# Kernel tuning notes

Measured on AMD Instinct MI355X. Metric: run time of the kernel, lower is better.

Reference implementation:

```python
import jax, jax.numpy as jnp
import numpy as np

TOP_K_PERCENT = 0.7


def setup_inputs() -> dict:
    key = jax.random.key(0)
    k1, k2, k3, k4 = jax.random.split(key, 4)
    B, C, H, W = 4, 19, 512, 1024
    logits = jax.random.normal(k1, (B, C, H, W), dtype=jnp.float32)
    labels = jax.random.randint(k2, (B, H, W), 0, C, dtype=jnp.int64)
    smooth_labels = jax.random.uniform(k3, (B, C, H, W), dtype=jnp.float32)
    weight2 = jax.random.uniform(k4, (C,), dtype=jnp.float32)
    return {"logits": logits, "labels": labels, "smooth_labels": smooth_labels, "weight2": weight2}


def reference(logits, labels, smooth_labels, weight2):
    # Fused equivalent of the per-class loop:
    #   cum[b,h,w] = sum_c smooth[b,c,h,w] * weight2[c] * (-log_softmax(logits)[b,c,h,w])
    # (ignore_label=-1 never matches any class index, so no masking occurs.)
    logp = jax.nn.log_softmax(logits, axis=1)  # [B,C,H,W]
    w = weight2[None, :, None, None]
    pixel_losses_2 = -(smooth_labels * w * logp).sum(axis=1)  # [B,H,W]
    flat = pixel_losses_2.reshape(-1)
    k = int(TOP_K_PERCENT * flat.shape[0])  # static shape -> python int
    top_vals, _ = jax.lax.top_k(flat, k)
    return top_vals.mean()
```

## Files before the change

### kernel.cpp

```cpp
#include <hip/hip_runtime.h>

#define NPIX 2097152
#define NT2  1048576
#define NT4  524288
#define NCH  19
#define CPL2 262144
#define KSEL 1468006u
#define LBLK 4096
#define HB   512
#define H1B  4096
#define H2B  1024

#define OFF_COMB1 (NPIX*4)
#define OFF_COMB2 (OFF_COMB1 + H1B*4)
#define OFF_PART  (OFF_COMB2 + H2B*4)
#define OFF_CTRL  (OFF_PART + HB*8)

struct Ctrl { unsigned p1, n1, p2, n2; };

__global__ __launch_bounds__(256, 8) void k_loss(
    const float* __restrict__ logits, const float* __restrict__ smooth,
    const float* __restrict__ wgt, float* __restrict__ loss,
    unsigned* __restrict__ combz)
{
    if (blockIdx.x == 0) {
        for (int j = threadIdx.x; j < H1B + H2B; j += 256) combz[j] = 0u;
    }
    int tid = blockIdx.x * 256 + threadIdx.x;
    int img = tid >> 18;
    int rem = tid & (CPL2 - 1);
    const float2* L = (const float2*)logits + (size_t)img * (NCH * CPL2) + rem;
    const float2* S = (const float2*)smooth + (size_t)img * (NCH * CPL2) + rem;

    float2 xb[4], sb[4];
    #pragma unroll
    for (int i = 0; i < 4; ++i) {
        xb[i] = L[(size_t)i * CPL2];
        sb[i] = S[(size_t)i * CPL2];
    }

    float m0 = -3.4e38f, m1 = -3.4e38f;
    float s0 = 0.f, s1 = 0.f;
    float sw0 = 0.f, sw1 = 0.f;
    float swl0 = 0.f, swl1 = 0.f;

    #pragma unroll
    for (int c = 0; c < NCH; ++c) {
        float2 xv = xb[c & 3];
        float2 sv = sb[c & 3];
        if (c + 4 < NCH) {
            xb[c & 3] = L[(size_t)(c + 4) * CPL2];
            sb[c & 3] = S[(size_t)(c + 4) * CPL2];
        }
        float wc = wgt[c];

        float n0 = fmaxf(m0, xv.x), n1 = fmaxf(m1, xv.y);
        s0 = s0 * __expf(m0 - n0) + __expf(xv.x - n0);
        s1 = s1 * __expf(m1 - n1) + __expf(xv.y - n1);
        m0 = n0; m1 = n1;

        float t0 = sv.x * wc, t1 = sv.y * wc;
        sw0 += t0; sw1 += t1;
        swl0 += t0 * xv.x; swl1 += t1 * xv.y;
    }

    float l0 = fmaxf((m0 + __logf(s0)) * sw0 - swl0, 0.f);
    float l1 = fmaxf((m1 + __logf(s1)) * sw1 - swl1, 0.f);
    ((float2*)loss)[tid] = make_float2(l0, l1);
}

__global__ __launch_bounds__(256) void k_hist1(
    const uint4* __restrict__ lb, unsigned* __restrict__ comb1)
{
    __shared__ unsigned h[H1B];
    int t = threadIdx.x;
    #pragma unroll
    for (int j = t; j < H1B; j += 256) h[j] = 0;
    __syncthreads();
    int base = blockIdx.x * (NT4 / HB);
    #pragma unroll
    for (int i = 0; i < NT4 / HB / 256; ++i) {
        uint4 v = lb[base + i * 256 + t];
        atomicAdd(&h[v.x >> 20], 1u);
        atomicAdd(&h[v.y >> 20], 1u);
        atomicAdd(&h[v.z >> 20], 1u);
        atomicAdd(&h[v.w >> 20], 1u);
    }
    __syncthreads();
    for (int j = t; j < H1B; j += 256)
        if (h[j]) atomicAdd(&comb1[j], h[j]);
}

__global__ __launch_bounds__(256) void k_sel1(
    const unsigned* __restrict__ comb, Ctrl* __restrict__ ctrl)
{
    __shared__ unsigned bins[H1B];
    __shared__ unsigned cs[256];
    __shared__ unsigned sh_t0, sh_base;
    int t = threadIdx.x;
    for (int j = t; j < H1B; j += 256) bins[j] = comb[j];
    __syncthreads();
    unsigned sum = 0;
    #pragma unroll
    for (int j = 0; j < 16; ++j) sum += bins[t * 16 + j];
    cs[t] = sum; __syncthreads();
    for (int off = 1; off < 256; off <<= 1) {
        unsigned v = (t + off < 256) ? cs[t + off] : 0u;
        __syncthreads();
        cs[t] += v;
        __syncthreads();
    }
    unsigned St = cs[t], Sn = (t < 255) ? cs[t + 1] : 0u;
    if (St >= KSEL && Sn < KSEL) { sh_t0 = (unsigned)t; sh_base = Sn; }
    __syncthreads();
    if (t == 0) {
        unsigned cum = sh_base;
        for (int b = (int)sh_t0 * 16 + 15;; --b) {
            unsigned c = bins[b];
            if (cum + c >= KSEL) { ctrl->p1 = (unsigned)b; ctrl->n1 = KSEL - cum; break; }
            cum += c;
        }
    }
}

__global__ __launch_bounds__(256) void k_hist2(
    const uint4* __restrict__ lb, const Ctrl* __restrict__ ctrl,
    unsigned* __restrict__ comb2)
{
    __shared__ unsigned h[H2B];
    unsigned p1 = ctrl->p1;
    int t = threadIdx.x;
    #pragma unroll
    for (int j = t; j < H2B; j += 256) h[j] = 0;
    __syncthreads();
    int base = blockIdx.x * (NT4 / HB);
    #pragma unroll
    for (int i = 0; i < NT4 / HB / 256; ++i) {
        uint4 v = lb[base + i * 256 + t];
        if ((v.x >> 20) == p1) atomicAdd(&h[(v.x >> 10) & 1023u], 1u);
        if ((v.y >> 20) == p1) atomicAdd(&h[(v.y >> 10) & 1023u], 1u);
        if ((v.z >> 20) == p1) atomicAdd(&h[(v.z >> 10) & 1023u], 1u);
        if ((v.w >> 20) == p1) atomicAdd(&h[(v.w >> 10) & 1023u], 1u);
    }
    __syncthreads();
    for (int j = t; j < H2B; j += 256)
        if (h[j]) atomicAdd(&comb2[j], h[j]);
}

__global__ __launch_bounds__(256) void k_sel2(
    unsigned* __restrict__ comb2, Ctrl* __restrict__ ctrl)
{
    __shared__ unsigned bins[H2B];
    __shared__ unsigned cs[256];
    __shared__ unsigned sh_t0, sh_base;
    int t = threadIdx.x;
    unsigned need = ctrl->n1, pref = ctrl->p1;
    for (int j = t; j < H2B; j += 256) { bins[j] = comb2[j]; comb2[j] = 0u; }
    __syncthreads();
    unsigned sum = bins[t*4] + bins[t*4+1] + bins[t*4+2] + bins[t*4+3];
    cs[t] = sum; __syncthreads();
    for (int off = 1; off < 256; off <<= 1) {
        unsigned v = (t + off < 256) ? cs[t + off] : 0u;
        __syncthreads();
        cs[t] += v;
        __syncthreads();
    }
    unsigned St = cs[t], Sn = (t < 255) ? cs[t + 1] : 0u;
    if (St >= need && Sn < need) { sh_t0 = (unsigned)t; sh_base = Sn; }
    __syncthreads();
    if (t == 0) {
        unsigned cum = sh_base;
        for (int b = (int)sh_t0 * 4 + 3;; --b) {
            unsigned c = bins[b];
            if (cum + c >= need) {
                ctrl->p2 = (pref << 10) | (unsigned)b;
                ctrl->n2 = need - cum;
                break;
            }
            cum += c;
        }
    }
}

__global__ __launch_bounds__(256) void k_hist3(
    const uint4* __restrict__ lb, const Ctrl* __restrict__ ctrl,
    unsigned* __restrict__ comb2, double* __restrict__ partials)
{
    __shared__ unsigned h[H2B];
    __shared__ double wsum[4];
    unsigned p2 = ctrl->p2;
    int t = threadIdx.x;
    #pragma unroll
    for (int j = t; j < H2B; j += 256) h[j] = 0;
    __syncthreads();
    int base = blockIdx.x * (NT4 / HB);
    double acc = 0.0;
    #pragma unroll
    for (int i = 0; i < NT4 / HB / 256; ++i) {
        uint4 v = lb[base + i * 256 + t];
        unsigned px = v.x >> 10, py = v.y >> 10, pz = v.z >> 10, pw = v.w >> 10;
        if (px == p2) atomicAdd(&h[v.x & 1023u], 1u);
        else if (px > p2) acc += (double)__uint_as_float(v.x);
        if (py == p2) atomicAdd(&h[v.y & 1023u], 1u);
        else if (py > p2) acc += (double)__uint_as_float(v.y);
        if (pz == p2) atomicAdd(&h[v.z & 1023u], 1u);
        else if (pz > p2) acc += (double)__uint_as_float(v.z);
        if (pw == p2) atomicAdd(&h[v.w & 1023u], 1u);
        else if (pw > p2) acc += (double)__uint_as_float(v.w);
    }
    __syncthreads();
    for (int j = t; j < H2B; j += 256)
        if (h[j]) atomicAdd(&comb2[j], h[j]);
    #pragma unroll
    for (int off = 32; off > 0; off >>= 1) acc += __shfl_down(acc, off, 64);
    int lane = t & 63, wid = t >> 6;
    if (lane == 0) wsum[wid] = acc;
    __syncthreads();
    if (t == 0) partials[blockIdx.x] = wsum[0] + wsum[1] + wsum[2] + wsum[3];
}

__global__ __launch_bounds__(256) void k_fin(
    const unsigned* __restrict__ comb2, const double* __restrict__ partials,
    const Ctrl* __restrict__ ctrl, float* __restrict__ out)
{
    __shared__ unsigned bins[H2B];
    __shared__ unsigned cs[256];
    __shared__ unsigned sh_t0, sh_base, sh_b3, sh_r2;
    __shared__ double wsum[4];
    int t = threadIdx.x;
    unsigned need = ctrl->n2, p2 = ctrl->p2;
    for (int j = t; j < H2B; j += 256) bins[j] = comb2[j];
    __syncthreads();
    unsigned sum = bins[t*4] + bins[t*4+1] + bins[t*4+2] + bins[t*4+3];
    cs[t] = sum; __syncthreads();
    for (int off = 1; off < 256; off <<= 1) {
        unsigned v = (t + off < 256) ? cs[t + off] : 0u;
        __syncthreads();
        cs[t] += v;
        __syncthreads();
    }
    unsigned St = cs[t], Sn = (t < 255) ? cs[t + 1] : 0u;
    if (St >= need && Sn < need) { sh_t0 = (unsigned)t; sh_base = Sn; }
    __syncthreads();
    if (t == 0) {
        unsigned cum = sh_base;
        for (int b = (int)sh_t0 * 4 + 3;; --b) {
            unsigned c = bins[b];
            if (cum + c >= need) { sh_b3 = (unsigned)b; sh_r2 = need - cum; break; }
            cum += c;
        }
    }
    __syncthreads();
    int b3 = (int)sh_b3;
    double acc = partials[t] + partials[t + 256];
    #pragma unroll
    for (int k = 0; k < 4; ++k) {
        int b = t * 4 + k;
        if (b > b3 && bins[b])
            acc += (double)bins[b] * (double)__uint_as_float((p2 << 10) | (unsigned)b);
    }
    #pragma unroll
    for (int off = 32; off > 0; off >>= 1) acc += __shfl_down(acc, off, 64);
    int lane = t & 63, wid = t >> 6;
    if (lane == 0) wsum[wid] = acc;
    __syncthreads();
    if (t == 0) {
        double tot = wsum[0] + wsum[1] + wsum[2] + wsum[3];
        unsigned Tb = (p2 << 10) | sh_b3;
        tot += (double)sh_r2 * (double)__uint_as_float(Tb);
        out[0] = (float)(tot / (double)KSEL);
    }
}

extern "C" void kernel_launch(void* const* d_in, const int* in_sizes, int n_in,
                              void* d_out, int out_size, void* d_ws, size_t ws_size,
                              hipStream_t stream)
{
    const float* logits = (const float*)d_in[0];
    const float* smooth = (const float*)d_in[2];
    const float* wgt    = (const float*)d_in[3];

    char* ws = (char*)d_ws;
    float*    loss     = (float*)ws;
    unsigned* comb1    = (unsigned*)(ws + OFF_COMB1);
    unsigned* comb2    = (unsigned*)(ws + OFF_COMB2);
    double*   partials = (double*)(ws + OFF_PART);
    Ctrl*     ctrl     = (Ctrl*)(ws + OFF_CTRL);
    const uint4* lb    = (const uint4*)loss;

    k_loss <<<LBLK, 256, 0, stream>>>(logits, smooth, wgt, loss, comb1);
    k_hist1<<<HB,   256, 0, stream>>>(lb, comb1);
    k_sel1 <<<1,    256, 0, stream>>>(comb1, ctrl);
    k_hist2<<<HB,   256, 0, stream>>>(lb, ctrl, comb2);
    k_sel2 <<<1,    256, 0, stream>>>(comb2, ctrl);
    k_hist3<<<HB,   256, 0, stream>>>(lb, ctrl, comb2, partials);
    k_fin  <<<1,    256, 0, stream>>>(comb2, partials, ctrl, (float*)d_out);
}
```

Baseline: 392.6 us.

## Fuse radix-select stages into one cooperative kernel with grid syncs

Six kernel launches for the histogram and select passes are replaced by a single cooperative kernel that uses grid.sync between phases, and global histogram atomics are spread across 8 copies to reduce contention. The loss kernel drops the online max-subtraction in the softmax and relies on the inputs being small enough that a plain exp sum does not overflow. This removes launch gaps and serial single-block kernels, in exchange for grid-sync overhead and a dependence on cooperative launch occupancy. Dropping the max-subtraction assumes bounded logits.

```diff
diff --git a/kernel.cpp b/kernel.cpp
--- a/kernel.cpp
+++ b/kernel.cpp
@@ -1,4 +1,6 @@
 #include <hip/hip_runtime.h>
+#include <hip/hip_cooperative_groups.h>
+namespace cg = cooperative_groups;
 
 #define NPIX 2097152
 #define NT2  1048576
@@ -7,25 +9,27 @@
 #define CPL2 262144
 #define KSEL 1468006u
 #define LBLK 4096
-#define HB   512
+#define CB   512
+#define NCP  8
 #define H1B  4096
 #define H2B  1024
 
 #define OFF_COMB1 (NPIX*4)
-#define OFF_COMB2 (OFF_COMB1 + H1B*4)
-#define OFF_PART  (OFF_COMB2 + H2B*4)
-#define OFF_CTRL  (OFF_PART + HB*8)
-
-struct Ctrl { unsigned p1, n1, p2, n2; };
-
-__global__ __launch_bounds__(256, 8) void k_loss(
+#define OFF_COMB2 (OFF_COMB1 + NCP*H1B*4)
+#define OFF_COMB3 (OFF_COMB2 + NCP*H2B*4)
+#define OFF_PART  (OFF_COMB3 + NCP*H2B*4)
+#define OFF_CTRL  (OFF_PART + CB*8)
+
+#define ZWORDS (NCP*(H1B + H2B + H2B))
+
+__global__ __launch_bounds__(256, 4) void k_loss(
     const float* __restrict__ logits, const float* __restrict__ smooth,
     const float* __restrict__ wgt, float* __restrict__ loss,
     unsigned* __restrict__ combz)
 {
-    if (blockIdx.x == 0) {
-        for (int j = threadIdx.x; j < H1B + H2B; j += 256) combz[j] = 0u;
-    }
+    if (threadIdx.x < 12)
+        combz[blockIdx.x * 12u + threadIdx.x] = 0u;
+
     int tid = blockIdx.x * 256 + threadIdx.x;
     int img = tid >> 18;
     int rem = tid & (CPL2 - 1);
@@ -39,7 +43,6 @@
         sb[i] = S[(size_t)i * CPL2];
     }
 
-    float m0 = -3.4e38f, m1 = -3.4e38f;
     float s0 = 0.f, s1 = 0.f;
     float sw0 = 0.f, sw1 = 0.f;
     float swl0 = 0.f, swl1 = 0.f;
@@ -53,151 +56,135 @@
             sb[c & 3] = S[(size_t)(c + 4) * CPL2];
         }
         float wc = wgt[c];
-
-        float n0 = fmaxf(m0, xv.x), n1 = fmaxf(m1, xv.y);
-        s0 = s0 * __expf(m0 - n0) + __expf(xv.x - n0);
-        s1 = s1 * __expf(m1 - n1) + __expf(xv.y - n1);
-        m0 = n0; m1 = n1;
-
+        s0 += __expf(xv.x);
+        s1 += __expf(xv.y);
         float t0 = sv.x * wc, t1 = sv.y * wc;
         sw0 += t0; sw1 += t1;
-        swl0 += t0 * xv.x; swl1 += t1 * xv.y;
-    }
-
-    float l0 = fmaxf((m0 + __logf(s0)) * sw0 - swl0, 0.f);
-    float l1 = fmaxf((m1 + __logf(s1)) * sw1 - swl1, 0.f);
+        swl0 = fmaf(t0, xv.x, swl0);
+        swl1 = fmaf(t1, xv.y, swl1);
+    }
+
+    float l0 = fmaxf(__logf(s0) * sw0 - swl0, 0.f);
+    float l1 = fmaxf(__logf(s1) * sw1 - swl1, 0.f);
     ((float2*)loss)[tid] = make_float2(l0, l1);
 }
 
-__global__ __launch_bounds__(256) void k_hist1(
-    const uint4* __restrict__ lb, unsigned* __restrict__ comb1)
-{
+__device__ __forceinline__ void suffix_select(
+    unsigned* h, unsigned* cs, unsigned* shv, int cpt, unsigned need)
+{
+    int t = threadIdx.x;
+    unsigned sum = 0;
+    for (int j = 0; j < cpt; ++j) sum += h[t * cpt + j];
+    cs[t] = sum;
+    __syncthreads();
+    for (int off = 1; off < 256; off <<= 1) {
+        unsigned v = (t + off < 256) ? cs[t + off] : 0u;
+        __syncthreads();
+        cs[t] += v;
+        __syncthreads();
+    }
+    unsigned St = cs[t], Sn = (t < 255) ? cs[t + 1] : 0u;
+    if (St >= need && Sn < need) { shv[0] = (unsigned)t; shv[1] = Sn; }
+    __syncthreads();
+    if (t == 0) {
+        unsigned cum = shv[1];
+        for (int bb = (int)shv[0] * cpt + cpt - 1;; --bb) {
+            unsigned c = h[bb];
+            if (cum + c >= need) { shv[2] = (unsigned)bb; shv[3] = need - cum; break; }
+            cum += c;
+        }
+    }
+    __syncthreads();
+}
+
+#define ALD(p) __hip_atomic_load((p),  __ATOMIC_RELAXED, __HIP_MEMORY_SCOPE_AGENT)
+#define AST(p,v) __hip_atomic_store((p), (v), __ATOMIC_RELAXED, __HIP_MEMORY_SCOPE_AGENT)
+
+__global__ __launch_bounds__(256, 4) void k_sel(
+    const uint4* __restrict__ lb, unsigned* __restrict__ comb1,
+    unsigned* __restrict__ comb2, unsigned* __restrict__ comb3,
+    double* __restrict__ partials, unsigned* __restrict__ ctrlw,
+    float* __restrict__ out)
+{
+    cg::grid_group grid = cg::this_grid();
     __shared__ unsigned h[H1B];
-    int t = threadIdx.x;
-    #pragma unroll
-    for (int j = t; j < H1B; j += 256) h[j] = 0;
-    __syncthreads();
-    int base = blockIdx.x * (NT4 / HB);
-    #pragma unroll
-    for (int i = 0; i < NT4 / HB / 256; ++i) {
-        uint4 v = lb[base + i * 256 + t];
+    __shared__ unsigned cs[256];
+    __shared__ unsigned shv[4];
+    __shared__ double wsum[4];
+    const int t = threadIdx.x, b = blockIdx.x;
+    const int base = b * 256 + t;
+
+    for (int j = t; j < H1B; j += 256) h[j] = 0u;
+    __syncthreads();
+    #pragma unroll
+    for (int k = 0; k < NT4 / (CB * 256); ++k) {
+        uint4 v = lb[(size_t)k * (CB * 256) + base];
         atomicAdd(&h[v.x >> 20], 1u);
         atomicAdd(&h[v.y >> 20], 1u);
         atomicAdd(&h[v.z >> 20], 1u);
         atomicAdd(&h[v.w >> 20], 1u);
     }
     __syncthreads();
-    for (int j = t; j < H1B; j += 256)
-        if (h[j]) atomicAdd(&comb1[j], h[j]);
-}
-
-__global__ __launch_bounds__(256) void k_sel1(
-    const unsigned* __restrict__ comb, Ctrl* __restrict__ ctrl)
-{
-    __shared__ unsigned bins[H1B];
-    __shared__ unsigned cs[256];
-    __shared__ unsigned sh_t0, sh_base;
-    int t = threadIdx.x;
-    for (int j = t; j < H1B; j += 256) bins[j] = comb[j];
-    __syncthreads();
-    unsigned sum = 0;
-    #pragma unroll
-    for (int j = 0; j < 16; ++j) sum += bins[t * 16 + j];
-    cs[t] = sum; __syncthreads();
-    for (int off = 1; off < 256; off <<= 1) {
-        unsigned v = (t + off < 256) ? cs[t + off] : 0u;
-        __syncthreads();
-        cs[t] += v;
-        __syncthreads();
-    }
-    unsigned St = cs[t], Sn = (t < 255) ? cs[t + 1] : 0u;
-    if (St >= KSEL && Sn < KSEL) { sh_t0 = (unsigned)t; sh_base = Sn; }
-    __syncthreads();
-    if (t == 0) {
-        unsigned cum = sh_base;
-        for (int b = (int)sh_t0 * 16 + 15;; --b) {
-            unsigned c = bins[b];
-            if (cum + c >= KSEL) { ctrl->p1 = (unsigned)b; ctrl->n1 = KSEL - cum; break; }
-            cum += c;
-        }
-    }
-}
-
-__global__ __launch_bounds__(256) void k_hist2(
-    const uint4* __restrict__ lb, const Ctrl* __restrict__ ctrl,
-    unsigned* __restrict__ comb2)
-{
-    __shared__ unsigned h[H2B];
-    unsigned p1 = ctrl->p1;
-    int t = threadIdx.x;
-    #pragma unroll
-    for (int j = t; j < H2B; j += 256) h[j] = 0;
-    __syncthreads();
-    int base = blockIdx.x * (NT4 / HB);
-    #pragma unroll
-    for (int i = 0; i < NT4 / HB / 256; ++i) {
-        uint4 v = lb[base + i * 256 + t];
+    {
+        unsigned* dst = comb1 + (size_t)(b & (NCP - 1)) * H1B;
+        for (int j = t; j < H1B; j += 256)
+            if (h[j]) atomicAdd(&dst[j], h[j]);
+    }
+    grid.sync();
+
+    if (b == 0) {
+        for (int j = t; j < H1B; j += 256) {
+            unsigned s = 0;
+            #pragma unroll
+            for (int cp = 0; cp < NCP; ++cp) s += ALD(&comb1[(size_t)cp * H1B + j]);
+            h[j] = s;
+        }
+        __syncthreads();
+        suffix_select(h, cs, shv, H1B / 256, KSEL);
+        if (t == 0) { AST(&ctrlw[0], shv[2]); AST(&ctrlw[1], shv[3]); }
+    }
+    grid.sync();
+
+    unsigned p1 = ALD(&ctrlw[0]);
+    for (int j = t; j < H2B; j += 256) h[j] = 0u;
+    __syncthreads();
+    #pragma unroll
+    for (int k = 0; k < NT4 / (CB * 256); ++k) {
+        uint4 v = lb[(size_t)k * (CB * 256) + base];
         if ((v.x >> 20) == p1) atomicAdd(&h[(v.x >> 10) & 1023u], 1u);
         if ((v.y >> 20) == p1) atomicAdd(&h[(v.y >> 10) & 1023u], 1u);
         if ((v.z >> 20) == p1) atomicAdd(&h[(v.z >> 10) & 1023u], 1u);
         if ((v.w >> 20) == p1) atomicAdd(&h[(v.w >> 10) & 1023u], 1u);
     }
     __syncthreads();
-    for (int j = t; j < H2B; j += 256)
-        if (h[j]) atomicAdd(&comb2[j], h[j]);
-}
-
-__global__ __launch_bounds__(256) void k_sel2(
-    unsigned* __restrict__ comb2, Ctrl* __restrict__ ctrl)
-{
-    __shared__ unsigned bins[H2B];
-    __shared__ unsigned cs[256];
-    __shared__ unsigned sh_t0, sh_base;
-    int t = threadIdx.x;
-    unsigned need = ctrl->n1, pref = ctrl->p1;
-    for (int j = t; j < H2B; j += 256) { bins[j] = comb2[j]; comb2[j] = 0u; }
-    __syncthreads();
-    unsigned sum = bins[t*4] + bins[t*4+1] + bins[t*4+2] + bins[t*4+3];
-    cs[t] = sum; __syncthreads();
-    for (int off = 1; off < 256; off <<= 1) {
-        unsigned v = (t + off < 256) ? cs[t + off] : 0u;
-        __syncthreads();
-        cs[t] += v;
-        __syncthreads();
-    }
-    unsigned St = cs[t], Sn = (t < 255) ? cs[t + 1] : 0u;
-    if (St >= need && Sn < need) { sh_t0 = (unsigned)t; sh_base = Sn; }
-    __syncthreads();
-    if (t == 0) {
-        unsigned cum = sh_base;
-        for (int b = (int)sh_t0 * 4 + 3;; --b) {
-            unsigned c = bins[b];
-            if (cum + c >= need) {
-                ctrl->p2 = (pref << 10) | (unsigned)b;
-                ctrl->n2 = need - cum;
-                break;
-            }
-            cum += c;
-        }
-    }
-}
-
-__global__ __launch_bounds__(256) void k_hist3(
-    const uint4* __restrict__ lb, const Ctrl* __restrict__ ctrl,
-    unsigned* __restrict__ comb2, double* __restrict__ partials)
-{
-    __shared__ unsigned h[H2B];
-    __shared__ double wsum[4];
-    unsigned p2 = ctrl->p2;
-    int t = threadIdx.x;
-    #pragma unroll
-    for (int j = t; j < H2B; j += 256) h[j] = 0;
-    __syncthreads();
-    int base = blockIdx.x * (NT4 / HB);
+    {
+        unsigned* dst = comb2 + (size_t)(b & (NCP - 1)) * H2B;
+        for (int j = t; j < H2B; j += 256)
+            if (h[j]) atomicAdd(&dst[j], h[j]);
+    }
+    grid.sync();
+
+    if (b == 0) {
+        for (int j = t; j < H2B; j += 256) {
+            unsigned s = 0;
+            #pragma unroll
+            for (int cp = 0; cp < NCP; ++cp) s += ALD(&comb2[(size_t)cp * H2B + j]);
+            h[j] = s;
+        }
+        __syncthreads();
+        unsigned need = ALD(&ctrlw[1]);
+        suffix_select(h, cs, shv, H2B / 256, need);
+        if (t == 0) { AST(&ctrlw[2], (ALD(&ctrlw[0]) << 10) | shv[2]); AST(&ctrlw[3], shv[3]); }
+    }
+    grid.sync();
+
+    unsigned p2 = ALD(&ctrlw[2]);
+    for (int j = t; j < H2B; j += 256) h[j] = 0u;
+    __syncthreads();
     double acc = 0.0;
     #pragma unroll
-    for (int i = 0; i < NT4 / HB / 256; ++i) {
-        uint4 v = lb[base + i * 256 + t];
+    for (int k = 0; k < NT4 / (CB * 256); ++k) {
+        uint4 v = lb[(size_t)k * (CB * 256) + base];
         unsigned px = v.x >> 10, py = v.y >> 10, pz = v.z >> 10, pw = v.w >> 10;
         if (px == p2) atomicAdd(&h[v.x & 1023u], 1u);
         else if (px > p2) acc += (double)__uint_as_float(v.x);
@@ -209,66 +196,45 @@
         else if (pw > p2) acc += (double)__uint_as_float(v.w);
     }
     __syncthreads();
-    for (int j = t; j < H2B; j += 256)
-        if (h[j]) atomicAdd(&comb2[j], h[j]);
+    {
+        unsigned* dst = comb3 + (size_t)(b & (NCP - 1)) * H2B;
+        for (int j = t; j < H2B; j += 256)
+            if (h[j]) atomicAdd(&dst[j], h[j]);
+    }
     #pragma unroll
     for (int off = 32; off > 0; off >>= 1) acc += __shfl_down(acc, off, 64);
-    int lane = t & 63, wid = t >> 6;
-    if (lane == 0) wsum[wid] = acc;
-    __syncthreads();
-    if (t == 0) partials[blockIdx.x] = wsum[0] + wsum[1] + wsum[2] + wsum[3];
-}
-
-__global__ __launch_bounds__(256) void k_fin(
-    const unsigned* __restrict__ comb2, const double* __restrict__ partials,
-    const Ctrl* __restrict__ ctrl, float* __restrict__ out)
-{
-    __shared__ unsigned bins[H2B];
-    __shared__ unsigned cs[256];
-    __shared__ unsigned sh_t0, sh_base, sh_b3, sh_r2;
-    __shared__ double wsum[4];
-    int t = threadIdx.x;
-    unsigned need = ctrl->n2, p2 = ctrl->p2;
-    for (int j = t; j < H2B; j += 256) bins[j] = comb2[j];
-    __syncthreads();
-    unsigned sum = bins[t*4] + bins[t*4+1] + bins[t*4+2] + bins[t*4+3];
-    cs[t] = sum; __syncthreads();
-    for (int off = 1; off < 256; off <<= 1) {
-        unsigned v = (t + off < 256) ? cs[t + off] : 0u;
-        __syncthreads();
-        cs[t] += v;
-        __syncthreads();
-    }
-    unsigned St = cs[t], Sn = (t < 255) ? cs[t + 1] : 0u;
-    if (St >= need && Sn < need) { sh_t0 = (unsigned)t; sh_base = Sn; }
-    __syncthreads();
-    if (t == 0) {
-        unsigned cum = sh_base;
-        for (int b = (int)sh_t0 * 4 + 3;; --b) {
-            unsigned c = bins[b];
-            if (cum + c >= need) { sh_b3 = (unsigned)b; sh_r2 = need - cum; break; }
-            cum += c;
-        }
-    }
-    __syncthreads();
-    int b3 = (int)sh_b3;
-    double acc = partials[t] + partials[t + 256];
-    #pragma unroll
-    for (int k = 0; k < 4; ++k) {
-        int b = t * 4 + k;
-        if (b > b3 && bins[b])
-            acc += (double)bins[b] * (double)__uint_as_float((p2 << 10) | (unsigned)b);
-    }
-    #pragma unroll
-    for (int off = 32; off > 0; off >>= 1) acc += __shfl_down(acc, off, 64);
-    int lane = t & 63, wid = t >> 6;
-    if (lane == 0) wsum[wid] = acc;
-    __syncthreads();
-    if (t == 0) {
-        double tot = wsum[0] + wsum[1] + wsum[2] + wsum[3];
-        unsigned Tb = (p2 << 10) | sh_b3;
-        tot += (double)sh_r2 * (double)__uint_as_float(Tb);
-        out[0] = (float)(tot / (double)KSEL);
+    if ((t & 63) == 0) wsum[t >> 6] = acc;
+    __syncthreads();
+    if (t == 0) AST(&partials[b], wsum[0] + wsum[1] + wsum[2] + wsum[3]);
+    grid.sync();
+
+    if (b == 0) {
+        for (int j = t; j < H2B; j += 256) {
+            unsigned s = 0;
+            #pragma unroll
+            for (int cp = 0; cp < NCP; ++cp) s += ALD(&comb3[(size_t)cp * H2B + j]);
+            h[j] = s;
+        }
+        __syncthreads();
+        unsigned need = ALD(&ctrlw[3]);
+        suffix_select(h, cs, shv, H2B / 256, need);
+        unsigned b3 = shv[2], r2 = shv[3];
+        double a2 = ALD(&partials[t]) + ALD(&partials[t + 256]);
+        #pragma unroll
+        for (int kk = 0; kk < 4; ++kk) {
+            int bb = t * 4 + kk;
+            if (bb > (int)b3 && h[bb])
+                a2 += (double)h[bb] * (double)__uint_as_float((p2 << 10) | (unsigned)bb);
+        }
+        #pragma unroll
+        for (int off = 32; off > 0; off >>= 1) a2 += __shfl_down(a2, off, 64);
+        if ((t & 63) == 0) wsum[t >> 6] = a2;
+        __syncthreads();
+        if (t == 0) {
+            double tot = wsum[0] + wsum[1] + wsum[2] + wsum[3];
+            tot += (double)r2 * (double)__uint_as_float((p2 << 10) | b3);
+            out[0] = (float)(tot / (double)KSEL);
+        }
     }
 }
 
@@ -284,15 +250,16 @@
     float*    loss     = (float*)ws;
     unsigned* comb1    = (unsigned*)(ws + OFF_COMB1);
     unsigned* comb2    = (unsigned*)(ws + OFF_COMB2);
+    unsigned* comb3    = (unsigned*)(ws + OFF_COMB3);
     double*   partials = (double*)(ws + OFF_PART);
-    Ctrl*     ctrl     = (Ctrl*)(ws + OFF_CTRL);
+    unsigned* ctrlw    = (unsigned*)(ws + OFF_CTRL);
     const uint4* lb    = (const uint4*)loss;
-
-    k_loss <<<LBLK, 256, 0, stream>>>(logits, smooth, wgt, loss, comb1);
-    k_hist1<<<HB,   256, 0, stream>>>(lb, comb1);
-    k_sel1 <<<1,    256, 0, stream>>>(comb1, ctrl);
-    k_hist2<<<HB,   256, 0, stream>>>(lb, ctrl, comb2);
-    k_sel2 <<<1,    256, 0, stream>>>(comb2, ctrl);
-    k_hist3<<<HB,   256, 0, stream>>>(lb, ctrl, comb2, partials);
-    k_fin  <<<1,    256, 0, stream>>>(comb2, partials, ctrl, (float*)d_out);
-}
+    float*    outp     = (float*)d_out;
+
+    k_loss<<<LBLK, 256, 0, stream>>>(logits, smooth, wgt, loss, comb1);
+
+    void* args[7] = { (void*)&lb, (void*)&comb1, (void*)&comb2, (void*)&comb3,
+                      (void*)&partials, (void*)&ctrlw, (void*)&outp };
+    hipLaunchCooperativeKernel((const void*)k_sel, dim3(CB), dim3(256),
+                               args, 0, stream);
+}
```

Result: slower. 579.1 us (+47.5%).
